# Performance work log

Measured on AMD Instinct MI355X. Metric: run time of the kernel, lower is better.

The kernel has to match this reference:

```python
import jax, jax.numpy as jnp
import numpy as np

B, S, D, H, E, K = 1, 4096, 1024, 4096, 8, 2


def setup_inputs() -> dict:
    key = jax.random.key(0)
    ks = jax.random.split(key, 10)
    scale = 0.02
    return {
        "hidden_states": jax.random.normal(ks[0], (B, S, D), dtype=jnp.float32),
        "gate_w": jax.random.normal(ks[1], (E, D), dtype=jnp.float32) * scale,
        "w_in": jax.random.normal(ks[2], (E, D, H), dtype=jnp.float32) * scale,
        "b_in": jnp.zeros((E, H), dtype=jnp.float32),
        "w_out": jax.random.normal(ks[3], (E, H, D), dtype=jnp.float32) * scale,
        "b_out": jnp.zeros((E, D), dtype=jnp.float32),
        "sw_in": jax.random.normal(ks[4], (D, H), dtype=jnp.float32) * scale,
        "sb_in": jnp.zeros((H,), dtype=jnp.float32),
        "sw_out": jax.random.normal(ks[5], (H, D), dtype=jnp.float32) * scale,
        "sb_out": jnp.zeros((D,), dtype=jnp.float32),
    }


def _ffn(x, w1, b1, w2, b2):
    # Linear -> exact (erf) GELU -> Linear, matching torch F.gelu default
    h = jax.nn.gelu(x @ w1 + b1, approximate=False)
    return h @ w2 + b2


def reference(hidden_states, gate_w, w_in, b_in, w_out, b_out,
              sw_in, sb_in, sw_out, sb_out):
    orig_shape = hidden_states.shape
    d = orig_shape[-1]
    x = hidden_states.reshape(-1, d)            # [T, D]
    T = x.shape[0]
    n_exp = gate_w.shape[0]

    # --- MoE gate: softmax over expert logits, top-k (sorted flag irrelevant
    # since the combine below is order-invariant) ---
    scores = jax.nn.softmax(x @ gate_w.T, axis=-1)        # [T, E]
    topk_w, topk_idx = jax.lax.top_k(scores, K)           # [T, K]

    # Per-token dense combine weights: w_tok[t, e] = sum of topk weights routed to e
    w_tok = jnp.zeros((T, n_exp), dtype=x.dtype).at[
        jnp.arange(T)[:, None], topk_idx].add(topk_w)     # [T, E]

    # --- expert dispatch + weighted combine (loop over small fixed E) ---
    y = jnp.zeros_like(x)
    for e in range(n_exp):
        y = y + w_tok[:, e:e + 1] * _ffn(x, w_in[e], b_in[e], w_out[e], b_out[e])

    # --- shared expert on the full (unflattened) input ---
    shared = _ffn(hidden_states, sw_in, sb_in, sw_out, sb_out)
    return y.reshape(orig_shape) + shared
```

## Files before the change

### kernel.cpp

```cpp
#include <hip/hip_runtime.h>
#include <hip/hip_bf16.h>
#include <math.h>


typedef unsigned short ushort_t;
typedef __attribute__((ext_vector_type(8))) __bf16 bf16x8;
typedef __attribute__((ext_vector_type(4))) float f32x4;

#define T_TOK 4096
#define DDIM  1024
#define HDIM  4096
#define NEXP  8
#define SLOT_PAD 10240
#define M_ALL (SLOT_PAD + T_TOK)

#define OFF_CNT   0u
#define OFF_OFFS  64u
#define OFF_TIDX  256u
#define OFF_TW    33024u
#define OFF_SLOT  65792u
#define OFF_TOK   98560u
#define OFF_XALL  1048576u
#define OFF_OUTS  OFF_XALL
#define OFF_WT    (OFF_XALL + 29360128u)
#define OFF_H     (OFF_WT + 75497472u)

__device__ __forceinline__ ushort_t f2b(float f) {
    __hip_bfloat16 h = __float2bfloat16(f);
    return *reinterpret_cast<ushort_t*>(&h);
}
__device__ __forceinline__ float b2f(ushort_t u) {
    __hip_bfloat16 h;
    *reinterpret_cast<ushort_t*>(&h) = u;
    return __bfloat162float(h);
}
__device__ __forceinline__ float gelu_fast(float v) {
    float u = 0.7978845608f * v * (1.0f + 0.044715f * v * v);
    float t = 1.0f - 2.0f / (__expf(2.0f * u) + 1.0f);
    return 0.5f * v * (1.0f + t);
}

__global__ void gate_kernel(const float* __restrict__ x, const float* __restrict__ gw,
                            int* __restrict__ tidx, float* __restrict__ tw,
                            int* __restrict__ cnt) {
    int t = blockIdx.x;
    int l = threadIdx.x;
    float acc[NEXP];
#pragma unroll
    for (int e = 0; e < NEXP; ++e) acc[e] = 0.f;
    for (int i = 0; i < DDIM / 64; ++i) {
        float xi = x[(size_t)t * DDIM + i * 64 + l];
#pragma unroll
        for (int e = 0; e < NEXP; ++e)
            acc[e] += xi * gw[e * DDIM + i * 64 + l];
    }
#pragma unroll
    for (int e = 0; e < NEXP; ++e)
        for (int off = 32; off; off >>= 1) acc[e] += __shfl_xor(acc[e], off);
    if (l == 0) {
        float m = acc[0];
#pragma unroll
        for (int e = 1; e < NEXP; ++e) m = fmaxf(m, acc[e]);
        float ex[NEXP], Z = 0.f;
#pragma unroll
        for (int e = 0; e < NEXP; ++e) { ex[e] = __expf(acc[e] - m); Z += ex[e]; }
        int b0 = 0;
#pragma unroll
        for (int e = 1; e < NEXP; ++e) if (ex[e] > ex[b0]) b0 = e;
        int b1 = (b0 == 0) ? 1 : 0;
#pragma unroll
        for (int e = 0; e < NEXP; ++e) if (e != b0 && ex[e] > ex[b1]) b1 = e;
        float inv = 1.0f / Z;
        tidx[2 * t] = b0; tidx[2 * t + 1] = b1;
        tw[2 * t] = ex[b0] * inv; tw[2 * t + 1] = ex[b1] * inv;
        atomicAdd(&cnt[b0], 1);
        atomicAdd(&cnt[b1], 1);
    }
}

__global__ void assign_kernel(const int* __restrict__ tidx, const int* __restrict__ cnt,
                              int* __restrict__ cur, int* __restrict__ offs,
                              int* __restrict__ slot_of, int* __restrict__ tok_of) {
    int off[NEXP + 1];
    off[0] = 0;
#pragma unroll
    for (int e = 0; e < NEXP; ++e) off[e + 1] = off[e] + ((cnt[e] + 255) & ~255);
    int i = blockIdx.x * 256 + threadIdx.x;
    if (i == 0) {
#pragma unroll
        for (int e = 0; e <= NEXP; ++e) offs[e] = off[e];
    }
    if (i >= 2 * T_TOK) return;
    int e = tidx[i];
    int s = off[e] + atomicAdd(&cur[e], 1);
    slot_of[i] = s;
    tok_of[s] = i >> 1;
}

__global__ void build_x(const float* __restrict__ x, const int* __restrict__ tok_of,
                        const int* __restrict__ offs, const int* __restrict__ cnt,
                        ushort_t* __restrict__ Xall) {
    int b = blockIdx.x;
    int k = threadIdx.x * 4;
    int t;
    if (b < SLOT_PAD) {
        if (b >= offs[NEXP]) return;
        int e = 0;
        while (offs[e + 1] <= b) e++;
        t = (b - offs[e] < cnt[e]) ? tok_of[b] : -1;
    } else {
        t = b - SLOT_PAD;
    }
    float4 v = make_float4(0.f, 0.f, 0.f, 0.f);
    if (t >= 0) v = *(const float4*)(x + (size_t)t * DDIM + k);
    ushort_t* p = Xall + (size_t)b * DDIM + k;
    p[0] = f2b(v.x); p[1] = f2b(v.y); p[2] = f2b(v.z); p[3] = f2b(v.w);
}

__global__ void transpose_cvt9(const float* __restrict__ w, const float* __restrict__ sw,
                               ushort_t* __restrict__ out, int K, int N) {
    __shared__ float t[64][65];
    int z = blockIdx.z;
    const float* in = (z < NEXP) ? w + (size_t)z * K * N : sw;
    out += (size_t)z * K * N;
    int k0 = blockIdx.x * 64, n0 = blockIdx.y * 64;
    int c = threadIdx.x & 63, r4 = threadIdx.x >> 6;
#pragma unroll
    for (int i = 0; i < 16; ++i) {
        int r = r4 + i * 4;
        t[r][c] = in[(size_t)(k0 + r) * N + n0 + c];
    }
    __syncthreads();
#pragma unroll
    for (int i = 0; i < 16; ++i) {
        int r = r4 + i * 4;
        out[(size_t)(n0 + r) * K + k0 + c] = f2b(t[c][r]);
    }
}

template <bool ACT_GELU, bool FFN2>
__global__ __launch_bounds__(1024, 4) void gemm_moe(
    const ushort_t* __restrict__ A, const ushort_t* __restrict__ WtBase,
    const float* __restrict__ bExp, const float* __restrict__ bSh,
    ushort_t* __restrict__ Cb, float* __restrict__ Cf,
    const int* __restrict__ offs, int N, int K) {
    int NMt = gridDim.x, NNt = gridDim.y;
    int flat = blockIdx.y * NMt + blockIdx.x;
    int xcd = flat & 7, rank = flat >> 3;
    int PM = NMt >> 2;
    int PN = NNt >> 1;
    int pm = xcd >> 1, pn = xcd & 1;
    int mi = pm * PM + rank / PN;
    int ni = pn * PN + rank % PN;
    int m0 = mi * 256, n0 = ni * 256;

    int e;
    if (m0 >= SLOT_PAD) {
        e = NEXP;
    } else {
        if (m0 >= offs[NEXP]) return;
        e = 0;
        while (offs[e + 1] <= m0) e++;
    }
    const ushort_t* Bt = WtBase + (size_t)e * N * K;
    const float* bias = (e == NEXP) ? bSh : bExp + (size_t)e * N;

    __shared__ ushort_t As[2][256 * 64];
    __shared__ ushort_t Bs[2][256 * 64];

    int tid = threadIdx.x;
    int lane = tid & 63, wid = tid >> 6;
    int wm = wid >> 2, wn = wid & 3;
    int q = lane >> 4, lr = lane & 15;

    size_t Aoff[2], Boff[2];
    int ldsOff[2];
#pragma unroll
    for (int it = 0; it < 2; ++it) {
        int L = it * 1024 + tid;
        int row = L >> 3;
        int c = (L & 7) ^ (row & 7);
        Aoff[it] = (size_t)(m0 + row) * K + c * 8;
        Boff[it] = (size_t)(n0 + row) * K + c * 8;
        ldsOff[it] = L * 8;
    }

    int rowA[4], rowB[4];
#pragma unroll
    for (int i = 0; i < 4; ++i) rowA[i] = wm * 64 + i * 16 + lr;
#pragma unroll
    for (int j = 0; j < 4; ++j) rowB[j] = wn * 64 + j * 16 + lr;

    f32x4 acc[4][4];
#pragma unroll
    for (int i = 0; i < 4; ++i)
#pragma unroll
        for (int j = 0; j < 4; ++j) acc[i][j] = (f32x4)(0.f);

    auto stage = [&](int kb, int buf) {
#pragma unroll
        for (int it = 0; it < 2; ++it) {
            __builtin_amdgcn_global_load_lds(
                (const __attribute__((address_space(1))) void*)(A + Aoff[it] + kb),
                (__attribute__((address_space(3))) void*)(&As[buf][ldsOff[it]]), 16, 0, 0);
            __builtin_amdgcn_global_load_lds(
                (const __attribute__((address_space(1))) void*)(Bt + Boff[it] + kb),
                (__attribute__((address_space(3))) void*)(&Bs[buf][ldsOff[it]]), 16, 0, 0);
        }
    };
    auto compute = [&](int buf) {
#pragma unroll
        for (int ks = 0; ks < 2; ++ks) {
            bf16x8 af[4], bfr[4];
#pragma unroll
            for (int i = 0; i < 4; ++i) {
                int cA = (ks * 4 + q) ^ (rowA[i] & 7);
                af[i] = *(const bf16x8*)(&As[buf][rowA[i] * 64 + cA * 8]);
            }
#pragma unroll
            for (int j = 0; j < 4; ++j) {
                int cB = (ks * 4 + q) ^ (rowB[j] & 7);
                bfr[j] = *(const bf16x8*)(&Bs[buf][rowB[j] * 64 + cB * 8]);
            }
#pragma unroll
            for (int i = 0; i < 4; ++i)
#pragma unroll
                for (int j = 0; j < 4; ++j)
                    acc[i][j] = __builtin_amdgcn_mfma_f32_16x16x32_bf16(
                        bfr[j], af[i], acc[i][j], 0, 0, 0);
        }
    };

    const int nk = K >> 6;
    stage(0, 0);
    int cur = 0;
    for (int t = 0; t < nk; ++t) {
        if (t + 1 < nk) {
            stage((t + 1) << 6, cur ^ 1);
            asm volatile("s_waitcnt vmcnt(4)" ::: "memory");
        } else {
            asm volatile("s_waitcnt vmcnt(0)" ::: "memory");
        }
        __builtin_amdgcn_s_barrier();
        compute(cur);
        __builtin_amdgcn_s_barrier();
        cur ^= 1;
    }

    int colb = n0 + wn * 64 + q * 4;
    int rowb = m0 + wm * 64 + lr;
    float4 bz[4];
#pragma unroll
    for (int nj = 0; nj < 4; ++nj)
        bz[nj] = *(const float4*)(bias + colb + nj * 16);
#pragma unroll
    for (int mi = 0; mi < 4; ++mi) {
        int row = rowb + mi * 16;
#pragma unroll
        for (int nj = 0; nj < 4; ++nj) {
            float v0 = acc[mi][nj][0] + bz[nj].x;
            float v1 = acc[mi][nj][1] + bz[nj].y;
            float v2 = acc[mi][nj][2] + bz[nj].z;
            float v3 = acc[mi][nj][3] + bz[nj].w;
            if (ACT_GELU) {
                v0 = gelu_fast(v0); v1 = gelu_fast(v1);
                v2 = gelu_fast(v2); v3 = gelu_fast(v3);
            }
            int col = colb + nj * 16;
            if (!FFN2 || e < NEXP) {
                uint2 u;
                u.x = (unsigned)f2b(v0) | ((unsigned)f2b(v1) << 16);
                u.y = (unsigned)f2b(v2) | ((unsigned)f2b(v3) << 16);
                *(uint2*)(Cb + (size_t)row * N + col) = u;
            } else {
                float4 f = make_float4(v0, v1, v2, v3);
                *(float4*)(Cf + (size_t)(row - SLOT_PAD) * N + col) = f;
            }
        }
    }
}

__global__ void combine_kernel(float* __restrict__ out, const ushort_t* __restrict__ OutS,
                               const int* __restrict__ slot_of, const float* __restrict__ tw) {
    int t = blockIdx.x;
    int d = threadIdx.x * 4;
    int s0 = slot_of[2 * t], s1 = slot_of[2 * t + 1];
    float w0 = tw[2 * t], w1 = tw[2 * t + 1];
    float* po = out + (size_t)t * DDIM + d;
    float4 o = *(float4*)po;
    const ushort_t* p0 = OutS + (size_t)s0 * DDIM + d;
    const ushort_t* p1 = OutS + (size_t)s1 * DDIM + d;
    o.x += w0 * b2f(p0[0]) + w1 * b2f(p1[0]);
    o.y += w0 * b2f(p0[1]) + w1 * b2f(p1[1]);
    o.z += w0 * b2f(p0[2]) + w1 * b2f(p1[2]);
    o.w += w0 * b2f(p0[3]) + w1 * b2f(p1[3]);
    *(float4*)po = o;
}

extern "C" void kernel_launch(void* const* d_in, const int* in_sizes, int n_in,
                              void* d_out, int out_size, void* d_ws, size_t ws_size,
                              hipStream_t stream) {
    const float* x      = (const float*)d_in[0];
    const float* gw     = (const float*)d_in[1];
    const float* w_in   = (const float*)d_in[2];
    const float* b_in   = (const float*)d_in[3];
    const float* w_out  = (const float*)d_in[4];
    const float* b_out  = (const float*)d_in[5];
    const float* sw_in  = (const float*)d_in[6];
    const float* sb_in  = (const float*)d_in[7];
    const float* sw_out = (const float*)d_in[8];
    const float* sb_out = (const float*)d_in[9];
    float* out = (float*)d_out;

    char* ws = (char*)d_ws;
    int*      cnt     = (int*)(ws + OFF_CNT);
    int*      offs    = (int*)(ws + OFF_OFFS);
    int*      tidx    = (int*)(ws + OFF_TIDX);
    float*    tw      = (float*)(ws + OFF_TW);
    int*      slot_of = (int*)(ws + OFF_SLOT);
    int*      tok_of  = (int*)(ws + OFF_TOK);
    ushort_t* Xall    = (ushort_t*)(ws + OFF_XALL);
    ushort_t* OutS    = (ushort_t*)(ws + OFF_OUTS);
    ushort_t* Wt      = (ushort_t*)(ws + OFF_WT);
    ushort_t* Hbuf    = (ushort_t*)(ws + OFF_H);

    hipMemsetAsync(cnt, 0, 64, stream);
    gate_kernel<<<T_TOK, 64, 0, stream>>>(x, gw, tidx, tw, cnt);
    assign_kernel<<<(2 * T_TOK + 255) / 256, 256, 0, stream>>>(tidx, cnt, cnt + 8,
                                                               offs, slot_of, tok_of);
    build_x<<<M_ALL, 256, 0, stream>>>(x, tok_of, offs, cnt, Xall);

    transpose_cvt9<<<dim3(DDIM / 64, HDIM / 64, NEXP + 1), 256, 0, stream>>>(
        w_in, sw_in, Wt, DDIM, HDIM);
    gemm_moe<true, false><<<dim3(M_ALL / 256, HDIM / 256), 1024, 0, stream>>>(
        Xall, Wt, b_in, sb_in, Hbuf, nullptr, offs, HDIM, DDIM);

    transpose_cvt9<<<dim3(HDIM / 64, DDIM / 64, NEXP + 1), 256, 0, stream>>>(
        w_out, sw_out, Wt, HDIM, DDIM);
    gemm_moe<false, true><<<dim3(M_ALL / 256, DDIM / 256), 1024, 0, stream>>>(
        Hbuf, Wt, b_out, sb_out, OutS, out, offs, DDIM, HDIM);

    combine_kernel<<<T_TOK, 256, 0, stream>>>(out, OutS, slot_of, tw);
    (void)in_sizes; (void)n_in; (void)out_size; (void)ws_size;
}
```

Before: 554.4 us.

## Shrink MoE GEMM tiles to 128x128x32 with 512-thread blocks

```diff
diff --git a/kernel.cpp b/kernel.cpp
--- a/kernel.cpp
+++ b/kernel.cpp
@@ -139,7 +139,7 @@
 }
 
 template <bool ACT_GELU, bool FFN2>
-__global__ __launch_bounds__(1024, 4) void gemm_moe(
+__global__ __launch_bounds__(512, 8) void gemm_moe(
     const ushort_t* __restrict__ A, const ushort_t* __restrict__ WtBase,
     const float* __restrict__ bExp, const float* __restrict__ bSh,
     ushort_t* __restrict__ Cb, float* __restrict__ Cf,
@@ -152,7 +152,7 @@
     int pm = xcd >> 1, pn = xcd & 1;
     int mi = pm * PM + rank / PN;
     int ni = pn * PN + rank % PN;
-    int m0 = mi * 256, n0 = ni * 256;
+    int m0 = mi * 128, n0 = ni * 128;
 
     int e;
     if (m0 >= SLOT_PAD) {
@@ -165,79 +165,63 @@
     const ushort_t* Bt = WtBase + (size_t)e * N * K;
     const float* bias = (e == NEXP) ? bSh : bExp + (size_t)e * N;
 
-    __shared__ ushort_t As[2][256 * 64];
-    __shared__ ushort_t Bs[2][256 * 64];
+    __shared__ ushort_t As[2][128 * 32];
+    __shared__ ushort_t Bs[2][128 * 32];
 
     int tid = threadIdx.x;
     int lane = tid & 63, wid = tid >> 6;
     int wm = wid >> 2, wn = wid & 3;
     int q = lane >> 4, lr = lane & 15;
 
-    size_t Aoff[2], Boff[2];
-    int ldsOff[2];
-#pragma unroll
-    for (int it = 0; it < 2; ++it) {
-        int L = it * 1024 + tid;
-        int row = L >> 3;
-        int c = (L & 7) ^ (row & 7);
-        Aoff[it] = (size_t)(m0 + row) * K + c * 8;
-        Boff[it] = (size_t)(n0 + row) * K + c * 8;
-        ldsOff[it] = L * 8;
-    }
-
-    int rowA[4], rowB[4];
-#pragma unroll
-    for (int i = 0; i < 4; ++i) rowA[i] = wm * 64 + i * 16 + lr;
-#pragma unroll
-    for (int j = 0; j < 4; ++j) rowB[j] = wn * 64 + j * 16 + lr;
-
-    f32x4 acc[4][4];
+    int srow = tid >> 2;
+    int su = ((tid & 3) ^ ((srow >> 1) & 3)) * 8;
+    size_t Aoff = (size_t)(m0 + srow) * K + su;
+    size_t Boff = (size_t)(n0 + srow) * K + su;
+    int ldsOff = tid * 8;
+
+    f32x4 acc[4][2];
 #pragma unroll
     for (int i = 0; i < 4; ++i)
 #pragma unroll
-        for (int j = 0; j < 4; ++j) acc[i][j] = (f32x4)(0.f);
+        for (int j = 0; j < 2; ++j) acc[i][j] = (f32x4)(0.f);
 
     auto stage = [&](int kb, int buf) {
-#pragma unroll
-        for (int it = 0; it < 2; ++it) {
-            __builtin_amdgcn_global_load_lds(
-                (const __attribute__((address_space(1))) void*)(A + Aoff[it] + kb),
-                (__attribute__((address_space(3))) void*)(&As[buf][ldsOff[it]]), 16, 0, 0);
-            __builtin_amdgcn_global_load_lds(
-                (const __attribute__((address_space(1))) void*)(Bt + Boff[it] + kb),
-                (__attribute__((address_space(3))) void*)(&Bs[buf][ldsOff[it]]), 16, 0, 0);
-        }
+        __builtin_amdgcn_global_load_lds(
+            (const __attribute__((address_space(1))) void*)(A + Aoff + kb),
+            (__attribute__((address_space(3))) void*)(&As[buf][ldsOff]), 16, 0, 0);
+        __builtin_amdgcn_global_load_lds(
+            (const __attribute__((address_space(1))) void*)(Bt + Boff + kb),
+            (__attribute__((address_space(3))) void*)(&Bs[buf][ldsOff]), 16, 0, 0);
     };
     auto compute = [&](int buf) {
-#pragma unroll
-        for (int ks = 0; ks < 2; ++ks) {
-            bf16x8 af[4], bfr[4];
-#pragma unroll
-            for (int i = 0; i < 4; ++i) {
-                int cA = (ks * 4 + q) ^ (rowA[i] & 7);
-                af[i] = *(const bf16x8*)(&As[buf][rowA[i] * 64 + cA * 8]);
-            }
-#pragma unroll
-            for (int j = 0; j < 4; ++j) {
-                int cB = (ks * 4 + q) ^ (rowB[j] & 7);
-                bfr[j] = *(const bf16x8*)(&Bs[buf][rowB[j] * 64 + cB * 8]);
-            }
-#pragma unroll
-            for (int i = 0; i < 4; ++i)
-#pragma unroll
-                for (int j = 0; j < 4; ++j)
-                    acc[i][j] = __builtin_amdgcn_mfma_f32_16x16x32_bf16(
-                        bfr[j], af[i], acc[i][j], 0, 0, 0);
+        bf16x8 af[4], bfr[2];
+#pragma unroll
+        for (int j = 0; j < 2; ++j) {
+            int r = wn * 32 + j * 16 + lr;
+            int c = q ^ ((r >> 1) & 3);
+            bfr[j] = *(const bf16x8*)(&Bs[buf][r * 32 + c * 8]);
         }
+#pragma unroll
+        for (int i = 0; i < 4; ++i) {
+            int r = wm * 64 + i * 16 + lr;
+            int c = q ^ ((r >> 1) & 3);
+            af[i] = *(const bf16x8*)(&As[buf][r * 32 + c * 8]);
+        }
+#pragma unroll
+        for (int i = 0; i < 4; ++i)
+#pragma unroll
+            for (int j = 0; j < 2; ++j)
+                acc[i][j] = __builtin_amdgcn_mfma_f32_16x16x32_bf16(
+                    bfr[j], af[i], acc[i][j], 0, 0, 0);
     };
 
-    const int nk = K >> 6;
+    const int nk = K >> 5;
     stage(0, 0);
     int cur = 0;
     for (int t = 0; t < nk; ++t) {
         if (t + 1 < nk) {
-            stage((t + 1) << 6, cur ^ 1);
-            asm volatile("s_waitcnt vmcnt(4)" ::: "memory");
+            stage((t + 1) << 5, cur ^ 1);
+            asm volatile("s_waitcnt vmcnt(2)" ::: "memory");
         } else {
             asm volatile("s_waitcnt vmcnt(0)" ::: "memory");
         }
@@ -247,17 +231,17 @@
         cur ^= 1;
     }
 
-    int colb = n0 + wn * 64 + q * 4;
+    int colb = n0 + wn * 32 + q * 4;
     int rowb = m0 + wm * 64 + lr;
-    float4 bz[4];
-#pragma unroll
-    for (int nj = 0; nj < 4; ++nj)
+    float4 bz[2];
+#pragma unroll
+    for (int nj = 0; nj < 2; ++nj)
         bz[nj] = *(const float4*)(bias + colb + nj * 16);
 #pragma unroll
     for (int mi = 0; mi < 4; ++mi) {
         int row = rowb + mi * 16;
 #pragma unroll
-        for (int nj = 0; nj < 4; ++nj) {
+        for (int nj = 0; nj < 2; ++nj) {
             float v0 = acc[mi][nj][0] + bz[nj].x;
             float v1 = acc[mi][nj][1] + bz[nj].y;
             float v2 = acc[mi][nj][2] + bz[nj].z;
@@ -332,12 +316,12 @@
 
     transpose_cvt9<<<dim3(DDIM / 64, HDIM / 64, NEXP + 1), 256, 0, stream>>>(
         w_in, sw_in, Wt, DDIM, HDIM);
-    gemm_moe<true, false><<<dim3(M_ALL / 256, HDIM / 256), 1024, 0, stream>>>(
+    gemm_moe<true, false><<<dim3(M_ALL / 128, HDIM / 128), 512, 0, stream>>>(
         Xall, Wt, b_in, sb_in, Hbuf, nullptr, offs, HDIM, DDIM);
 
     transpose_cvt9<<<dim3(HDIM / 64, DDIM / 64, NEXP + 1), 256, 0, stream>>>(
         w_out, sw_out, Wt, HDIM, DDIM);
-    gemm_moe<false, true><<<dim3(M_ALL / 256, DDIM / 256), 1024, 0, stream>>>(
+    gemm_moe<false, true><<<dim3(M_ALL / 128, DDIM / 128), 512, 0, stream>>>(
         Hbuf, Wt, b_out, sb_out, OutS, out, offs, DDIM, HDIM);
 
     combine_kernel<<<T_TOK, 256, 0, stream>>>(out, OutS, slot_of, tw);
```

New measurement: 564.7 us. About the same (+1.9%).
